# Kernel optimization log

Measured on AMD Instinct MI355X. Metric: run time of the kernel, lower is better.

Reference implementation:

```python
import jax, jax.numpy as jnp
import numpy as np

T, B, E, H, R = 1024, 8, 1024, 16, 16
HD = E // H


def setup_inputs() -> dict:
    key = jax.random.key(0)
    ks = jax.random.split(key, 10)
    w = lambda k, shape: (jax.random.normal(k, shape, jnp.float32) * 0.02)
    return {
        "query": jax.random.normal(ks[0], (T, B, E), jnp.float32),
        "in_proj_weight": w(ks[1], (3 * E, E)),
        "in_proj_bias": jnp.zeros((3 * E,), jnp.float32),
        "in_left": w(ks[2], (3 * E, R)),   # LrkLinear(rank -> 3E) weight
        "in_right": w(ks[3], (R, E)),      # LrkLinear(E -> rank) weight
        "out_proj_weight": w(ks[4], (E, E)),
        "out_proj_bias": jnp.zeros((E,), jnp.float32),
        "out_left": w(ks[5], (E, R)),
        "out_right": w(ks[6], (R, E)),
        "rel_pos_bias": w(ks[7], (H, T, T)),
    }


def reference(query, in_proj_weight, in_proj_bias, in_left, in_right,
              out_proj_weight, out_proj_bias, out_left, out_right, rel_pos_bias):
    t, b, e = query.shape
    hd = e // H
    scaling = float(hd) ** -0.5
    # fused in-projection: residual full-rank + low-rank branch
    acti = (jnp.einsum('tbe,fe->tbf', query, in_proj_weight) + in_proj_bias
            + jnp.einsum('tbr,fr->tbf', jnp.einsum('tbe,re->tbr', query, in_right), in_left))
    q, k, v = jnp.split(acti, 3, axis=-1)
    q = q * scaling
    # (T,B,E) -> (B,H,T,hd); matches torch view(T, B*H, hd).transpose(0,1)
    to_heads = lambda x: x.reshape(t, b, H, hd).transpose(1, 2, 0, 3)
    qh, kh, vh = to_heads(q), to_heads(k), to_heads(v)
    scores = jnp.einsum('bhtd,bhsd->bhts', qh, kh) + rel_pos_bias  # bias broadcasts over batch
    attn = jax.nn.softmax(scores, axis=-1)  # dropout_p = 0
    out = jnp.einsum('bhts,bhsd->bhtd', attn, vh)
    out = out.transpose(2, 0, 1, 3).reshape(t, b, e)
    # out-projection: residual full-rank + low-rank branch
    out = (jnp.einsum('tbe,fe->tbf', out, out_proj_weight) + out_proj_bias
           + jnp.einsum('tbr,fr->tbf', jnp.einsum('tbe,re->tbr', out, out_right), out_left))
    return out
```

## Files before the change

kernel.cpp:

```cpp
#include <hip/hip_runtime.h>
#include <hip/hip_bf16.h>


typedef __attribute__((ext_vector_type(8))) __bf16 bf16x8;
typedef __attribute__((ext_vector_type(4))) float f32x4;

#define LOG2E 1.44269504f

__device__ __forceinline__ float bf2f(unsigned short u) {
  union { unsigned int i; float f; } v; v.i = ((unsigned int)u) << 16; return v.f;
}
__device__ __forceinline__ unsigned short f2bf(float f) {
  union { float f; unsigned int i; } v; v.f = f;
  unsigned int x = v.i;
  unsigned int r = x + 0x7FFFu + ((x >> 16) & 1u);
  return (unsigned short)(r >> 16);
}
__device__ __forceinline__ unsigned int pack2(float a, float b) {
  return (unsigned int)f2bf(a) | ((unsigned int)f2bf(b) << 16);
}
__device__ __forceinline__ float ld_in(const void* p, long idx, int isf32) {
  if (isf32) return ((const float*)p)[idx];
  return bf2f(((const unsigned short*)p)[idx]);
}
__device__ __forceinline__ float fexp2(float x) {
#if __has_builtin(__builtin_amdgcn_exp2f)
  return __builtin_amdgcn_exp2f(x);
#else
  return __expf(x * 0.69314718056f);
#endif
}
__device__ __forceinline__ void gl_lds16(const unsigned short* g, unsigned short* l) {
  __builtin_amdgcn_global_load_lds(
      (const __attribute__((address_space(1))) unsigned int*)g,
      (__attribute__((address_space(3))) unsigned int*)l, 16, 0, 0);
}

__global__ void detect_kernel(const unsigned int* __restrict__ q, int* __restrict__ flag) {
  __shared__ int cnt;
  if (threadIdx.x == 0) cnt = 0;
  __syncthreads();
  unsigned int w = q[threadIdx.x];
  int c = 0;
  if (((w >> 7) & 0xFFu) >= 0xC0u) c++;
  if (((w >> 23) & 0xFFu) >= 0xC0u) c++;
  atomicAdd(&cnt, c);
  __syncthreads();
  if (threadIdx.x == 0) flag[0] = (cnt >= 2) ? 1 : 0;
}

__global__ __launch_bounds__(256) void convert_bias(
    const void* __restrict__ in, unsigned short* __restrict__ out,
    const int* __restrict__ flag) {
  long idx = ((long)blockIdx.x * 256 + threadIdx.x) * 8;
  if (flag[0]) {
    const float* p = (const float*)in + idx;
    float4 a = ((const float4*)p)[0], b = ((const float4*)p)[1];
    uint4 v;
    v.x = pack2(a.x * LOG2E, a.y * LOG2E); v.y = pack2(a.z * LOG2E, a.w * LOG2E);
    v.z = pack2(b.x * LOG2E, b.y * LOG2E); v.w = pack2(b.z * LOG2E, b.w * LOG2E);
    *(uint4*)(out + idx) = v;
  } else {
    const unsigned short* p = (const unsigned short*)in + idx;
    unsigned short s[8];
#pragma unroll
    for (int i = 0; i < 8; ++i) s[i] = f2bf(bf2f(p[i]) * LOG2E);
    uint4 v;
    v.x = (unsigned int)s[0] | ((unsigned int)s[1] << 16);
    v.y = (unsigned int)s[2] | ((unsigned int)s[3] << 16);
    v.z = (unsigned int)s[4] | ((unsigned int)s[5] << 16);
    v.w = (unsigned int)s[6] | ((unsigned int)s[7] << 16);
    *(uint4*)(out + idx) = v;
  }
}

__global__ __launch_bounds__(256) void convert_q(
    const void* __restrict__ in, unsigned short* __restrict__ out,
    const int* __restrict__ flag) {
  long idx = ((long)blockIdx.x * 256 + threadIdx.x) * 8;
  const int inrow = (int)(idx >> 10);
  const int e = (int)(idx & 1023);
  const long oidx = ((long)((inrow & 7) << 10 | (inrow >> 3))) * 1024 + e;
  if (flag[0]) {
    const float* p = (const float*)in + idx;
    float4 a = ((const float4*)p)[0], b = ((const float4*)p)[1];
    uint4 v;
    v.x = pack2(a.x, a.y); v.y = pack2(a.z, a.w);
    v.z = pack2(b.x, b.y); v.w = pack2(b.z, b.w);
    *(uint4*)(out + oidx) = v;
  } else {
    *(uint4*)(out + oidx) = *(const uint4*)((const unsigned short*)in + idx);
  }
}

__global__ __launch_bounds__(256) void eff_weights(
    const void* __restrict__ w, const void* __restrict__ left,
    const void* __restrict__ right, unsigned short* __restrict__ outw,
    const int* __restrict__ flag) {
  const int isf32 = flag[0];
  long idx = (long)blockIdx.x * 256 + threadIdx.x;
  long f = idx >> 10, e = idx & 1023;
  float acc = ld_in(w, idx, isf32);
#pragma unroll
  for (int r = 0; r < 16; ++r)
    acc += ld_in(left, (f << 4) + r, isf32) * ld_in(right, (r << 10) + e, isf32);
  outw[idx] = f2bf(acc);
}

__global__ __launch_bounds__(256) void inproj_kernel(
    const unsigned short* __restrict__ qbf,
    const unsigned short* __restrict__ weff,
    const void* __restrict__ bias,
    unsigned short* __restrict__ qh, unsigned short* __restrict__ kh,
    unsigned short* __restrict__ vt, const int* __restrict__ flag) {
  __shared__ __align__(16) unsigned short As[2 * 128 * 32];
  __shared__ __align__(16) unsigned short Bs[2 * 128 * 32];
  const int isf32 = flag[0];
  const int tid = threadIdx.x;
  const int wave = tid >> 6, lane = tid & 63, quad = lane >> 4, lrow = lane & 15;
  const int wr0 = (wave >> 1) * 64, wc0 = (wave & 1) * 64;
  const int fbase = blockIdx.x * 128, mbase = blockIdx.y * 128;
  const int srow = lane >> 2, scol = (lane & 3) * 8;
  const unsigned short* ag  = qbf  + (long)(mbase + 32 * wave + srow) * 1024 + scol;
  const unsigned short* ag2 = ag + 16 * 1024;
  const unsigned short* bg  = weff + (long)(fbase + 32 * wave + srow) * 1024 + scol;
  const unsigned short* bg2 = bg + 16 * 1024;
  unsigned short* la  = &As[(32 * wave) * 32];
  unsigned short* la2 = &As[(32 * wave + 16) * 32];
  unsigned short* lb  = &Bs[(32 * wave) * 32];
  unsigned short* lb2 = &Bs[(32 * wave + 16) * 32];

  f32x4 acc[4][4] = {};
  for (int k0 = 0; k0 < 1024; k0 += 64) {
    gl_lds16(ag + k0, la);
    gl_lds16(ag2 + k0, la2);
    gl_lds16(ag + k0 + 32, la + 4096);
    gl_lds16(ag2 + k0 + 32, la2 + 4096);
    gl_lds16(bg + k0, lb);
    gl_lds16(bg2 + k0, lb2);
    gl_lds16(bg + k0 + 32, lb + 4096);
    gl_lds16(bg2 + k0 + 32, lb2 + 4096);
    __syncthreads();
#pragma unroll
    for (int kk = 0; kk < 2; ++kk) {
      bf16x8 af[4], bfv[4];
#pragma unroll
      for (int mi = 0; mi < 4; ++mi)
        af[mi] = *(const bf16x8*)&As[kk * 4096 + (wr0 + mi * 16 + lrow) * 32 + quad * 8];
#pragma unroll
      for (int ni = 0; ni < 4; ++ni)
        bfv[ni] = *(const bf16x8*)&Bs[kk * 4096 + (wc0 + ni * 16 + lrow) * 32 + quad * 8];
#pragma unroll
      for (int mi = 0; mi < 4; ++mi)
#pragma unroll
        for (int ni = 0; ni < 4; ++ni)
          acc[mi][ni] = __builtin_amdgcn_mfma_f32_16x16x32_bf16(af[mi], bfv[ni], acc[mi][ni], 0, 0, 0);
    }
    __syncthreads();
  }
  const int which = fbase >> 10;
  const int h = ((fbase + wc0) >> 6) & 15;
  const int bq = mbase >> 10;
  const int tbase = (mbase & 1023) + wr0;
#pragma unroll
  for (int ni = 0; ni < 4; ++ni) {
    const int d = ni * 16 + lrow;
    const float bv = ld_in(bias, fbase + wc0 + d, isf32);
    if (which == 2) {
      unsigned short* vrow = vt + ((long)(bq * 16 + h) * 64 + d) * 1024;
#pragma unroll
      for (int mi = 0; mi < 4; ++mi) {
        const int t = tbase + mi * 16 + quad * 4;
        ushort4 v;
        v.x = f2bf(acc[mi][ni][0] + bv);
        v.y = f2bf(acc[mi][ni][1] + bv);
        v.z = f2bf(acc[mi][ni][2] + bv);
        v.w = f2bf(acc[mi][ni][3] + bv);
        *(ushort4*)(vrow + t) = v;
      }
    } else {
      unsigned short* qk = (which == 0) ? qh : kh;
      const float sc = (which == 0) ? (0.125f * LOG2E) : 1.0f;
      unsigned short* row0 = qk + (long)(bq * 16 + h) * 65536;
#pragma unroll
      for (int mi = 0; mi < 4; ++mi)
#pragma unroll
        for (int r = 0; r < 4; ++r) {
          const int t = tbase + mi * 16 + quad * 4 + r;
          row0[(long)t * 64 + d] = f2bf((acc[mi][ni][r] + bv) * sc);
        }
    }
  }
}

__global__ __launch_bounds__(512) void attn_kernel(
    const unsigned short* __restrict__ qh, const unsigned short* __restrict__ kh,
    const unsigned short* __restrict__ vt, const void* __restrict__ rpb,
    const unsigned short* __restrict__ pre,
    unsigned short* __restrict__ ctx, const int* __restrict__ flag) {
  __shared__ __align__(16) unsigned short Ks[2][4096];
  __shared__ __align__(16) unsigned short Vs[2][4096];
  __shared__ __align__(16) unsigned short Ps[8][1024];
  const int isf32 = flag[0];
  const int tid = threadIdx.x;
  const int wave = tid >> 6, lane = tid & 63, quad = lane >> 4, lrow = lane & 15;
  const int b = blockIdx.y & 7, h = blockIdx.y >> 3, bh = b * 16 + h;
  const int t0 = blockIdx.x * 128;

  const unsigned short* qbase = qh + ((long)(bh * 1024) + t0 + wave * 16 + lrow) * 64;
  bf16x8 qf0 = *(const bf16x8*)(qbase + quad * 8);
  bf16x8 qf1 = *(const bf16x8*)(qbase + 32 + quad * 8);

  const unsigned short* kbase = kh + (long)bh * 65536;
  const unsigned short* vbase = vt + (long)bh * 65536;

  const long bidx0 = ((long)h * 1024 + t0 + wave * 16 + quad * 4) * 1024 + lrow;
  const unsigned short* bs16 = pre ? pre : (const unsigned short*)rpb;
  const bool bf32 = (isf32 && pre == nullptr);
  const bool prescaled = (pre != nullptr);
  const float* bsf = (const float*)rpb;

  const int kkj = wave >> 2, iij = wave & 3;
  const int sr = lane >> 2, sc = (lane & 3) * 8;
  const unsigned short* kg = kbase + (long)(16 * iij + sr) * 64 + kkj * 32 + sc;
  const unsigned short* vg = vbase + (long)(16 * iij + sr) * 1024 + kkj * 32 + sc;
  const int lo = kkj * 2048 + iij * 512;

  f32x4 oacc[4] = {};
  float rsum[4] = {0.f, 0.f, 0.f, 0.f};
  unsigned int bcur[4][4], bnxt[4][4];

  gl_lds16(kg, &Ks[0][lo]);
  gl_lds16(vg, &Vs[0][lo]);
  if (bf32) {
#pragma unroll
    for (int r = 0; r < 4; ++r)
#pragma unroll
      for (int n = 0; n < 4; ++n)
        bcur[r][n] = __float_as_uint(bsf[bidx0 + r * 1024 + n * 16]);
  } else {
#pragma unroll
    for (int r = 0; r < 4; ++r)
#pragma unroll
      for (int n = 0; n < 4; ++n)
        bcur[r][n] = (unsigned int)bs16[bidx0 + r * 1024 + n * 16];
  }
  __syncthreads();

  for (int t = 0; t < 16; ++t) {
    const int cur = t & 1;
    const int s0 = t << 6;
    if (t < 15) {
      const int sn = s0 + 64;
      gl_lds16(kg + (long)sn * 64, &Ks[cur ^ 1][lo]);
      gl_lds16(vg + sn, &Vs[cur ^ 1][lo]);
      if (bf32) {
#pragma unroll
        for (int r = 0; r < 4; ++r)
#pragma unroll
          for (int n = 0; n < 4; ++n)
            bnxt[r][n] = __float_as_uint(bsf[bidx0 + r * 1024 + sn + n * 16]);
      } else {
#pragma unroll
        for (int r = 0; r < 4; ++r)
#pragma unroll
          for (int n = 0; n < 4; ++n)
            bnxt[r][n] = (unsigned int)bs16[bidx0 + r * 1024 + sn + n * 16];
      }
    }

    f32x4 sacc[4] = {};
#pragma unroll
    for (int n = 0; n < 4; ++n) {
      bf16x8 kf0 = *(const bf16x8*)&Ks[cur][(n * 16 + lrow) * 32 + quad * 8];
      bf16x8 kf1 = *(const bf16x8*)&Ks[cur][2048 + (n * 16 + lrow) * 32 + quad * 8];
      sacc[n] = __builtin_amdgcn_mfma_f32_16x16x32_bf16(qf0, kf0, sacc[n], 0, 0, 0);
      sacc[n] = __builtin_amdgcn_mfma_f32_16x16x32_bf16(qf1, kf1, sacc[n], 0, 0, 0);
    }

#pragma unroll
    for (int n = 0; n < 4; ++n)
#pragma unroll
      for (int rr = 0; rr < 2; ++rr) {
        const int r0 = 2 * rr, r1 = r0 + 1;
        float b0, b1;
        if (bf32) { b0 = __uint_as_float(bcur[r0][n]); b1 = __uint_as_float(bcur[r1][n]); }
        else      { b0 = bf2f((unsigned short)bcur[r0][n]); b1 = bf2f((unsigned short)bcur[r1][n]); }
        float x0, x1;
        if (prescaled) { x0 = sacc[n][r0] + b0; x1 = sacc[n][r1] + b1; }
        else { x0 = __builtin_fmaf(b0, LOG2E, sacc[n][r0]); x1 = __builtin_fmaf(b1, LOG2E, sacc[n][r1]); }
        const float p0 = fexp2(x0), p1 = fexp2(x1);
        rsum[r0] += p0; rsum[r1] += p1;
        unsigned int u;
        asm("v_cvt_pk_bf16_f32 %0, %1, %2" : "=v"(u) : "v"(p0), "v"(p1));
        const int row0 = quad * 4 + r0, row1 = row0 + 1;
        Ps[wave][(row0 * 64 + n * 16 + lrow) ^ ((row0 & 7) << 3)] = (unsigned short)u;
        Ps[wave][(row1 * 64 + n * 16 + lrow) ^ ((row1 & 7) << 3)] = (unsigned short)(u >> 16);
      }

    asm volatile("s_waitcnt lgkmcnt(0)" ::: "memory");

#pragma unroll
    for (int kk = 0; kk < 2; ++kk) {
      bf16x8 pf = *(const bf16x8*)&Ps[wave][(lrow * 64 + kk * 32 + quad * 8) ^ ((lrow & 7) << 3)];
#pragma unroll
      for (int n = 0; n < 4; ++n) {
        bf16x8 vf = *(const bf16x8*)&Vs[cur][kk * 2048 + (n * 16 + lrow) * 32 + quad * 8];
        oacc[n] = __builtin_amdgcn_mfma_f32_16x16x32_bf16(pf, vf, oacc[n], 0, 0, 0);
      }
    }
    __syncthreads();
    if (t < 15) {
#pragma unroll
      for (int r = 0; r < 4; ++r)
#pragma unroll
        for (int n = 0; n < 4; ++n) bcur[r][n] = bnxt[r][n];
    }
  }

#pragma unroll
  for (int msk = 1; msk <= 8; msk <<= 1)
#pragma unroll
    for (int r = 0; r < 4; ++r)
      rsum[r] += __shfl_xor(rsum[r], msk, 64);

  float linv[4];
#pragma unroll
  for (int r = 0; r < 4; ++r) linv[r] = 1.0f / rsum[r];
#pragma unroll
  for (int n = 0; n < 4; ++n)
#pragma unroll
    for (int r = 0; r < 4; ++r) {
      const int t = t0 + wave * 16 + quad * 4 + r;
      ctx[((long)t * 8 + b) * 1024 + h * 64 + n * 16 + lrow] = f2bf(oacc[n][r] * linv[r]);
    }
}

__global__ __launch_bounds__(256) void outproj_kernel(
    const unsigned short* __restrict__ ctx, const unsigned short* __restrict__ weff,
    const void* __restrict__ bias, void* __restrict__ out,
    const int* __restrict__ flag) {
  __shared__ __align__(16) unsigned short As[2 * 128 * 32];
  __shared__ __align__(16) unsigned short Bs[2 * 128 * 32];
  const int isf32 = flag[0];
  const int tid = threadIdx.x;
  const int wave = tid >> 6, lane = tid & 63, quad = lane >> 4, lrow = lane & 15;
  const int wr0 = (wave >> 1) * 64, wc0 = (wave & 1) * 64;
  const int fbase = blockIdx.x * 128, mbase = blockIdx.y * 128;
  const int srow = lane >> 2, scol = (lane & 3) * 8;
  const unsigned short* ag  = ctx  + (long)(mbase + 32 * wave + srow) * 1024 + scol;
  const unsigned short* ag2 = ag + 16 * 1024;
  const unsigned short* bg  = weff + (long)(fbase + 32 * wave + srow) * 1024 + scol;
  const unsigned short* bg2 = bg + 16 * 1024;
  unsigned short* la  = &As[(32 * wave) * 32];
  unsigned short* la2 = &As[(32 * wave + 16) * 32];
  unsigned short* lb  = &Bs[(32 * wave) * 32];
  unsigned short* lb2 = &Bs[(32 * wave + 16) * 32];

  f32x4 acc[4][4] = {};
  for (int k0 = 0; k0 < 1024; k0 += 64) {
    gl_lds16(ag + k0, la);
    gl_lds16(ag2 + k0, la2);
    gl_lds16(ag + k0 + 32, la + 4096);
    gl_lds16(ag2 + k0 + 32, la2 + 4096);
    gl_lds16(bg + k0, lb);
    gl_lds16(bg2 + k0, lb2);
    gl_lds16(bg + k0 + 32, lb + 4096);
    gl_lds16(bg2 + k0 + 32, lb2 + 4096);
    __syncthreads();
#pragma unroll
    for (int kk = 0; kk < 2; ++kk) {
      bf16x8 af[4], bfv[4];
#pragma unroll
      for (int mi = 0; mi < 4; ++mi)
        af[mi] = *(const bf16x8*)&As[kk * 4096 + (wr0 + mi * 16 + lrow) * 32 + quad * 8];
#pragma unroll
      for (int ni = 0; ni < 4; ++ni)
        bfv[ni] = *(const bf16x8*)&Bs[kk * 4096 + (wc0 + ni * 16 + lrow) * 32 + quad * 8];
#pragma unroll
      for (int mi = 0; mi < 4; ++mi)
#pragma unroll
        for (int ni = 0; ni < 4; ++ni)
          acc[mi][ni] = __builtin_amdgcn_mfma_f32_16x16x32_bf16(af[mi], bfv[ni], acc[mi][ni], 0, 0, 0);
    }
    __syncthreads();
  }
#pragma unroll
  for (int ni = 0; ni < 4; ++ni) {
    const int f = fbase + wc0 + ni * 16 + lrow;
    const float bv = ld_in(bias, f, isf32);
#pragma unroll
    for (int mi = 0; mi < 4; ++mi)
#pragma unroll
      for (int r = 0; r < 4; ++r) {
        const int m = mbase + wr0 + mi * 16 + quad * 4 + r;
        const float val = acc[mi][ni][r] + bv;
        if (isf32) ((float*)out)[(long)m * 1024 + f] = val;
        else       ((unsigned short*)out)[(long)m * 1024 + f] = f2bf(val);
      }
  }
}

extern "C" void kernel_launch(void* const* d_in, const int* in_sizes, int n_in,
                              void* d_out, int out_size, void* d_ws, size_t ws_size,
                              hipStream_t stream) {
  (void)out_size;
  static const int EXP[10] = {8388608, 3145728, 3072, 49152, 16384,
                              1048576, 1024, 16384, 16384, 16777216};
  if (n_in != 10) return;
  for (int i = 0; i < 10; ++i) if (in_sizes[i] != EXP[i]) return;

  const void* query = d_in[0];
  const void* ipw = d_in[1];  const void* ipb = d_in[2];
  const void* il  = d_in[3];  const void* ir  = d_in[4];
  const void* opw = d_in[5];  const void* opb = d_in[6];
  const void* ol  = d_in[7];  const void* orr = d_in[8];
  const void* rpb = d_in[9];

  int* flag = (int*)d_ws;
  unsigned short* base = (unsigned short*)d_ws + 16;
  unsigned short* w_in_eff  = base;
  unsigned short* w_out_eff = w_in_eff + (long)3072 * 1024;
  unsigned short* qh  = w_out_eff + (long)1024 * 1024;
  unsigned short* kh  = qh + 8388608L;
  unsigned short* vt  = kh + 8388608L;
  unsigned short* ctx = vt + 8388608L;
  unsigned short* rpbbf = ctx + 8388608L;
  unsigned short* qbf = ctx;
  const size_t NEED_FULL = 32 + (3145728L + 1048576L + 4L * 8388608L + 16777216L) * 2;
  const bool big = ws_size >= NEED_FULL;

  detect_kernel<<<dim3(1), dim3(64), 0, stream>>>((const unsigned int*)query, flag);
  if (big)
    convert_bias<<<dim3(8192), dim3(256), 0, stream>>>(rpb, rpbbf, flag);
  convert_q<<<dim3(4096), dim3(256), 0, stream>>>(query, qbf, flag);
  eff_weights<<<dim3(12288), dim3(256), 0, stream>>>(ipw, il, ir, w_in_eff, flag);
  eff_weights<<<dim3(4096), dim3(256), 0, stream>>>(opw, ol, orr, w_out_eff, flag);
  inproj_kernel<<<dim3(24, 64), dim3(256), 0, stream>>>(qbf, w_in_eff, ipb, qh, kh, vt, flag);
  attn_kernel<<<dim3(8, 128), dim3(512), 0, stream>>>(qh, kh, vt, rpb,
                                                      big ? rpbbf : nullptr, ctx, flag);
  outproj_kernel<<<dim3(8, 64), dim3(256), 0, stream>>>(ctx, w_out_eff, opb, d_out, flag);
}
```

Baseline: 396.5 us.

## Double KV tile to 128 keys per barrier and swizzle block order

```diff
diff --git a/kernel.cpp b/kernel.cpp
--- a/kernel.cpp
+++ b/kernel.cpp
@@ -198,14 +198,17 @@
     const unsigned short* __restrict__ vt, const void* __restrict__ rpb,
     const unsigned short* __restrict__ pre,
     unsigned short* __restrict__ ctx, const int* __restrict__ flag) {
-  __shared__ __align__(16) unsigned short Ks[2][4096];
-  __shared__ __align__(16) unsigned short Vs[2][4096];
+  __shared__ __align__(16) unsigned short Ks[2][8192];
+  __shared__ __align__(16) unsigned short Vs[2][8192];
   __shared__ __align__(16) unsigned short Ps[8][1024];
   const int isf32 = flag[0];
   const int tid = threadIdx.x;
   const int wave = tid >> 6, lane = tid & 63, quad = lane >> 4, lrow = lane & 15;
-  const int b = blockIdx.y & 7, h = blockIdx.y >> 3, bh = b * 16 + h;
-  const int t0 = blockIdx.x * 128;
+  const int dl = blockIdx.x + (blockIdx.y << 3);
+  const int g = dl >> 6, r_ = dl & 63;
+  const int w = (g << 6) | ((r_ & 7) << 3) | (r_ >> 3);
+  const int b = (w >> 3) & 7, h = w >> 6, bh = b * 16 + h;
+  const int t0 = (w & 7) * 128;
 
   const unsigned short* qbase = qh + ((long)(bh * 1024) + t0 + wave * 16 + lrow) * 64;
   bf16x8 qf0 = *(const bf16x8*)(qbase + quad * 8);
@@ -220,18 +223,25 @@
   const bool prescaled = (pre != nullptr);
   const float* bsf = (const float*)rpb;
 
-  const int kkj = wave >> 2, iij = wave & 3;
   const int sr = lane >> 2, sc = (lane & 3) * 8;
-  const unsigned short* kg = kbase + (long)(16 * iij + sr) * 64 + kkj * 32 + sc;
-  const unsigned short* vg = vbase + (long)(16 * iij + sr) * 1024 + kkj * 32 + sc;
-  const int lo = kkj * 2048 + iij * 512;
+  const int j0 = 2 * wave, j1 = j0 + 1;
+  const int kkA = j0 >> 3, iiA = j0 & 7, kkB = j1 >> 3, iiB = j1 & 7;
+  const int ssA = j0 & 3, ddA = j0 >> 2, ssB = j1 & 3, ddB = j1 >> 2;
+  const unsigned short* kgA = kbase + (long)(16 * iiA + sr) * 64 + kkA * 32 + sc;
+  const unsigned short* kgB = kbase + (long)(16 * iiB + sr) * 64 + kkB * 32 + sc;
+  const unsigned short* vgA = vbase + (long)(16 * ddA + sr) * 1024 + ssA * 32 + sc;
+  const unsigned short* vgB = vbase + (long)(16 * ddB + sr) * 1024 + ssB * 32 + sc;
+  const int kloA = kkA * 4096 + iiA * 512, kloB = kkB * 4096 + iiB * 512;
+  const int vloA = ssA * 2048 + ddA * 512, vloB = ssB * 2048 + ddB * 512;
 
   f32x4 oacc[4] = {};
   float rsum[4] = {0.f, 0.f, 0.f, 0.f};
   unsigned int bcur[4][4], bnxt[4][4];
 
-  gl_lds16(kg, &Ks[0][lo]);
-  gl_lds16(vg, &Vs[0][lo]);
+  gl_lds16(kgA, &Ks[0][kloA]);
+  gl_lds16(kgB, &Ks[0][kloB]);
+  gl_lds16(vgA, &Vs[0][vloA]);
+  gl_lds16(vgB, &Vs[0][vloB]);
   if (bf32) {
 #pragma unroll
     for (int r = 0; r < 4; ++r)
@@ -247,75 +257,84 @@
   }
   __syncthreads();
 
-  for (int t = 0; t < 16; ++t) {
+  for (int t = 0; t < 8; ++t) {
     const int cur = t & 1;
-    const int s0 = t << 6;
-    if (t < 15) {
-      const int sn = s0 + 64;
-      gl_lds16(kg + (long)sn * 64, &Ks[cur ^ 1][lo]);
-      gl_lds16(vg + sn, &Vs[cur ^ 1][lo]);
-      if (bf32) {
+    const int s0 = t << 7;
+    if (t < 7) {
+      const int sn = s0 + 128;
+      gl_lds16(kgA + (long)sn * 64, &Ks[cur ^ 1][kloA]);
+      gl_lds16(kgB + (long)sn * 64, &Ks[cur ^ 1][kloB]);
+      gl_lds16(vgA + sn, &Vs[cur ^ 1][vloA]);
+      gl_lds16(vgB + sn, &Vs[cur ^ 1][vloB]);
+    }
+#pragma unroll
+    for (int hh = 0; hh < 2; ++hh) {
+      f32x4 sacc[4] = {};
+#pragma unroll
+      for (int n = 0; n < 4; ++n) {
+        const int srow_ = (hh * 64 + n * 16 + lrow) * 32 + quad * 8;
+        bf16x8 kf0 = *(const bf16x8*)&Ks[cur][srow_];
+        bf16x8 kf1 = *(const bf16x8*)&Ks[cur][4096 + srow_];
+        sacc[n] = __builtin_amdgcn_mfma_f32_16x16x32_bf16(qf0, kf0, sacc[n], 0, 0, 0);
+        sacc[n] = __builtin_amdgcn_mfma_f32_16x16x32_bf16(qf1, kf1, sacc[n], 0, 0, 0);
+      }
+      const int hnext = 2 * t + hh + 1;
+      if (hnext <= 15) {
+        const int cn = hnext * 64;
+        if (bf32) {
+#pragma unroll
+          for (int r = 0; r < 4; ++r)
+#pragma unroll
+            for (int n = 0; n < 4; ++n)
+              bnxt[r][n] = __float_as_uint(bsf[bidx0 + r * 1024 + cn + n * 16]);
+        } else {
+#pragma unroll
+          for (int r = 0; r < 4; ++r)
+#pragma unroll
+            for (int n = 0; n < 4; ++n)
+              bnxt[r][n] = (unsigned int)bs16[bidx0 + r * 1024 + cn + n * 16];
+        }
+      }
+#pragma unroll
+      for (int n = 0; n < 4; ++n)
+#pragma unroll
+        for (int rr = 0; rr < 2; ++rr) {
+          const int r0 = 2 * rr, r1 = r0 + 1;
+          float b0, b1;
+          if (bf32) { b0 = __uint_as_float(bcur[r0][n]); b1 = __uint_as_float(bcur[r1][n]); }
+          else      { b0 = bf2f((unsigned short)bcur[r0][n]); b1 = bf2f((unsigned short)bcur[r1][n]); }
+          float x0, x1;
+          if (prescaled) { x0 = sacc[n][r0] + b0; x1 = sacc[n][r1] + b1; }
+          else { x0 = __builtin_fmaf(b0, LOG2E, sacc[n][r0]); x1 = __builtin_fmaf(b1, LOG2E, sacc[n][r1]); }
+          const float p0 = fexp2(x0), p1 = fexp2(x1);
+          rsum[r0] += p0; rsum[r1] += p1;
+          unsigned int u;
+          asm("v_cvt_pk_bf16_f32 %0, %1, %2" : "=v"(u) : "v"(p0), "v"(p1));
+          const int row0 = quad * 4 + r0, row1 = row0 + 1;
+          Ps[wave][(row0 * 64 + n * 16 + lrow) ^ ((row0 & 7) << 3)] = (unsigned short)u;
+          Ps[wave][(row1 * 64 + n * 16 + lrow) ^ ((row1 & 7) << 3)] = (unsigned short)(u >> 16);
+        }
+
+      asm volatile("s_waitcnt lgkmcnt(0)" ::: "memory");
+
+#pragma unroll
+      for (int kkk = 0; kkk < 2; ++kkk) {
+        bf16x8 pf = *(const bf16x8*)&Ps[wave][(lrow * 64 + kkk * 32 + quad * 8) ^ ((lrow & 7) << 3)];
+        const int chunk = hh * 2 + kkk;
+#pragma unroll
+        for (int n = 0; n < 4; ++n) {
+          bf16x8 vf = *(const bf16x8*)&Vs[cur][chunk * 2048 + (n * 16 + lrow) * 32 + quad * 8];
+          oacc[n] = __builtin_amdgcn_mfma_f32_16x16x32_bf16(pf, vf, oacc[n], 0, 0, 0);
+        }
+      }
+      if (hnext <= 15) {
 #pragma unroll
         for (int r = 0; r < 4; ++r)
 #pragma unroll
-          for (int n = 0; n < 4; ++n)
-            bnxt[r][n] = __float_as_uint(bsf[bidx0 + r * 1024 + sn + n * 16]);
-      } else {
-#pragma unroll
-        for (int r = 0; r < 4; ++r)
-#pragma unroll
-          for (int n = 0; n < 4; ++n)
-            bnxt[r][n] = (unsigned int)bs16[bidx0 + r * 1024 + sn + n * 16];
-      }
-    }
-
-    f32x4 sacc[4] = {};
-#pragma unroll
-    for (int n = 0; n < 4; ++n) {
-      bf16x8 kf0 = *(const bf16x8*)&Ks[cur][(n * 16 + lrow) * 32 + quad * 8];
-      bf16x8 kf1 = *(const bf16x8*)&Ks[cur][2048 + (n * 16 + lrow) * 32 + quad * 8];
-      sacc[n] = __builtin_amdgcn_mfma_f32_16x16x32_bf16(qf0, kf0, sacc[n], 0, 0, 0);
-      sacc[n] = __builtin_amdgcn_mfma_f32_16x16x32_bf16(qf1, kf1, sacc[n], 0, 0, 0);
-    }
-
-#pragma unroll
-    for (int n = 0; n < 4; ++n)
-#pragma unroll
-      for (int rr = 0; rr < 2; ++rr) {
-        const int r0 = 2 * rr, r1 = r0 + 1;
-        float b0, b1;
-        if (bf32) { b0 = __uint_as_float(bcur[r0][n]); b1 = __uint_as_float(bcur[r1][n]); }
-        else      { b0 = bf2f((unsigned short)bcur[r0][n]); b1 = bf2f((unsigned short)bcur[r1][n]); }
-        float x0, x1;
-        if (prescaled) { x0 = sacc[n][r0] + b0; x1 = sacc[n][r1] + b1; }
-        else { x0 = __builtin_fmaf(b0, LOG2E, sacc[n][r0]); x1 = __builtin_fmaf(b1, LOG2E, sacc[n][r1]); }
-        const float p0 = fexp2(x0), p1 = fexp2(x1);
-        rsum[r0] += p0; rsum[r1] += p1;
-        unsigned int u;
-        asm("v_cvt_pk_bf16_f32 %0, %1, %2" : "=v"(u) : "v"(p0), "v"(p1));
-        const int row0 = quad * 4 + r0, row1 = row0 + 1;
-        Ps[wave][(row0 * 64 + n * 16 + lrow) ^ ((row0 & 7) << 3)] = (unsigned short)u;
-        Ps[wave][(row1 * 64 + n * 16 + lrow) ^ ((row1 & 7) << 3)] = (unsigned short)(u >> 16);
-      }
-
-    asm volatile("s_waitcnt lgkmcnt(0)" ::: "memory");
-
-#pragma unroll
-    for (int kk = 0; kk < 2; ++kk) {
-      bf16x8 pf = *(const bf16x8*)&Ps[wave][(lrow * 64 + kk * 32 + quad * 8) ^ ((lrow & 7) << 3)];
-#pragma unroll
-      for (int n = 0; n < 4; ++n) {
-        bf16x8 vf = *(const bf16x8*)&Vs[cur][kk * 2048 + (n * 16 + lrow) * 32 + quad * 8];
-        oacc[n] = __builtin_amdgcn_mfma_f32_16x16x32_bf16(pf, vf, oacc[n], 0, 0, 0);
+          for (int n = 0; n < 4; ++n) bcur[r][n] = bnxt[r][n];
       }
     }
     __syncthreads();
-    if (t < 15) {
-#pragma unroll
-      for (int r = 0; r < 4; ++r)
-#pragma unroll
-        for (int n = 0; n < 4; ++n) bcur[r][n] = bnxt[r][n];
-    }
   }
 
 #pragma unroll
```

Result: slower. 404.4 us (+2.0%).
